# Kernel optimization log

Hardware: AMD Instinct MI355X
Metric: run time of the kernel (lower is better)

## Reference

```python
import jax, jax.numpy as jnp
import numpy as np

N_NODES = 100000
N_EDGES = 1600000
IN_FEATS = 512
HEADS = 8
HID = 8            # out_feats per head of the input layer
N_CLASSES = 40
NEG_SLOPE = 0.2    # DGL GATv2Conv default


def gatv2_layer(h, src, dst, Ws, bs, Wd, bd, attn, n_nodes):
    """One DGL-style GATv2Conv (eval mode: dropouts are identity).
    h: [N, F_in]; Ws/Wd: [F_in, H*D]; attn: [H, D]. Returns [N, H*D]."""
    H, D = attn.shape
    hs = (h @ Ws + bs).reshape(-1, H, D)   # fc_src(h)
    hd = (h @ Wd + bd).reshape(-1, H, D)   # fc_dst(h)
    es = hs[src]                           # [E,H,D] messages (feat_src on edges)
    ed = hd[dst]                           # [E,H,D]
    e = jax.nn.leaky_relu(es + ed, NEG_SLOPE)
    logits = jnp.einsum('ehd,hd->eh', e, attn)          # [E,H]
    # segment softmax over incoming edges of each dst node
    m = jax.ops.segment_max(logits, dst, num_segments=n_nodes)
    m = jnp.where(jnp.isfinite(m), m, 0.0)              # nodes with no in-edges
    p = jnp.exp(logits - m[dst])
    s = jax.ops.segment_sum(p, dst, num_segments=n_nodes)
    alpha = p / (s[dst] + 1e-9)                         # [E,H]
    out = jax.ops.segment_sum(alpha[:, :, None] * es, dst, num_segments=n_nodes)
    return out.reshape(n_nodes, H * D)


def setup_inputs() -> dict:
    key = jax.random.key(0)
    ks = jax.random.split(key, 12)
    x = jax.random.normal(ks[0], (N_NODES, IN_FEATS), dtype=jnp.float32)
    src = jax.random.randint(ks[1], (N_EDGES,), 0, N_NODES, dtype=jnp.int32)
    dst = jax.random.randint(ks[2], (N_EDGES,), 0, N_NODES, dtype=jnp.int32)
    s1 = 1.0 / np.sqrt(IN_FEATS)
    s2 = 1.0 / np.sqrt(HEADS * HID)
    W1s = jax.random.normal(ks[3], (IN_FEATS, HEADS * HID), dtype=jnp.float32) * s1
    W1d = jax.random.normal(ks[4], (IN_FEATS, HEADS * HID), dtype=jnp.float32) * s1
    b1s = jnp.zeros((HEADS * HID,), jnp.float32)
    b1d = jnp.zeros((HEADS * HID,), jnp.float32)
    a1 = jax.random.normal(ks[5], (HEADS, HID), dtype=jnp.float32) * s2
    W2s = jax.random.normal(ks[6], (HEADS * HID, N_CLASSES), dtype=jnp.float32) * s2
    W2d = jax.random.normal(ks[7], (HEADS * HID, N_CLASSES), dtype=jnp.float32) * s2
    b2s = jnp.zeros((N_CLASSES,), jnp.float32)
    b2d = jnp.zeros((N_CLASSES,), jnp.float32)
    a2 = jax.random.normal(ks[8], (1, N_CLASSES), dtype=jnp.float32) * (1.0 / np.sqrt(N_CLASSES))
    return {"x": x, "src": src, "dst": dst,
            "W1s": W1s, "b1s": b1s, "W1d": W1d, "b1d": b1d, "a1": a1,
            "W2s": W2s, "b2s": b2s, "W2d": W2d, "b2d": b2d, "a2": a2}


def reference(x, src, dst, W1s, b1s, W1d, b1d, a1, W2s, b2s, W2d, b2d, a2):
    h = gatv2_layer(x, src, dst, W1s, b1s, W1d, b1d, a1, N_NODES)   # [N, H*HID]
    h = jax.nn.elu(h)
    out = gatv2_layer(h, src, dst, W2s, b2s, W2d, b2d, a2, N_NODES)  # [N, C]
    return out
```

## Files before the change

### kernel.cpp

```cpp
#include <hip/hip_runtime.h>
#include <math.h>

#define N_NODES 100000
#define N_EDGES 1600000
#define F_IN    512
#define HD1     64
#define NHEAD   8
#define NC      40
#define NEG_SLOPE 0.2f

typedef _Float16 h8 __attribute__((ext_vector_type(8)));
typedef _Float16 h4 __attribute__((ext_vector_type(4)));
typedef float f4 __attribute__((ext_vector_type(4)));

__global__ __launch_bounds__(256) void prep_all(
    const float* __restrict__ W1s, const float* __restrict__ W1d,
    _Float16* __restrict__ btgf,
    const float* __restrict__ W2s, const float* __restrict__ W2d,
    _Float16* __restrict__ btg2, int* __restrict__ deg){
  int i = blockIdx.x*256 + threadIdx.x;
  {
    int j = i & 7, lane = (i>>3)&63, t = (i>>9)&7, kstep = i>>12;
    int k = kstep*32 + (lane>>4)*8 + j;
    int n = t*16 + (lane&15);
    float v = (n < 64) ? W1s[k*64 + n] : W1d[k*64 + (n-64)];
    btgf[i] = (_Float16)v;
  }
  if(i < 80*64){
    int n = i >> 6, k = i & 63;
    float v = (n < 40) ? W2s[k*40 + n] : W2d[k*40 + (n-40)];
    btg2[i] = (_Float16)v;
  }
  for(int k=i; k<N_NODES; k+=65536) deg[k] = 0;
}

__global__ __launch_bounds__(256) void hist_dst(const int* __restrict__ dst,
                                                int* __restrict__ deg){
  int xcd = blockIdx.x & 7;
  int lo = xcd*12500, hi = lo + 12500;
  int e0 = (blockIdx.x >> 3)*1024 + threadIdx.x*4;
  if(e0 + 3 < N_EDGES){
    int4 d4 = *(const int4*)&dst[e0];
    if(d4.x >= lo && d4.x < hi) atomicAdd(&deg[d4.x], 1);
    if(d4.y >= lo && d4.y < hi) atomicAdd(&deg[d4.y], 1);
    if(d4.z >= lo && d4.z < hi) atomicAdd(&deg[d4.z], 1);
    if(d4.w >= lo && d4.w < hi) atomicAdd(&deg[d4.w], 1);
  } else {
    for(int j=0;j<4;j++){
      int e = e0 + j;
      if(e < N_EDGES){
        int d = dst[e];
        if(d >= lo && d < hi) atomicAdd(&deg[d], 1);
      }
    }
  }
}

__global__ __launch_bounds__(256) void scan1(const int* __restrict__ deg,
                                             int* __restrict__ row,
                                             int* __restrict__ bsum){
  __shared__ int sm[256];
  int t = threadIdx.x;
  int base = blockIdx.x*1024 + t*4;
  int v0 = base+0<N_NODES ? deg[base+0] : 0;
  int v1 = base+1<N_NODES ? deg[base+1] : 0;
  int v2 = base+2<N_NODES ? deg[base+2] : 0;
  int v3 = base+3<N_NODES ? deg[base+3] : 0;
  int tsum = v0+v1+v2+v3;
  sm[t] = tsum; __syncthreads();
  for(int off=1; off<256; off<<=1){
    int x = (t>=off) ? sm[t-off] : 0;
    __syncthreads();
    sm[t] += x;
    __syncthreads();
  }
  int excl = sm[t] - tsum;
  if(t==255) bsum[blockIdx.x] = sm[255];
  if(base+0<N_NODES) row[base+0] = excl;
  if(base+1<N_NODES) row[base+1] = excl+v0;
  if(base+2<N_NODES) row[base+2] = excl+v0+v1;
  if(base+3<N_NODES) row[base+3] = excl+v0+v1+v2;
}

__global__ __launch_bounds__(128) void scan2(int* __restrict__ bsum, int nb){
  __shared__ int sm[128];
  int t = threadIdx.x;
  int v = (t<nb) ? bsum[t] : 0;
  sm[t] = v; __syncthreads();
  for(int off=1; off<128; off<<=1){
    int x = (t>=off) ? sm[t-off] : 0;
    __syncthreads();
    sm[t] += x;
    __syncthreads();
  }
  if(t<nb) bsum[t] = sm[t] - v;
}

__global__ __launch_bounds__(256) void scan3(int* __restrict__ row,
                                             const int* __restrict__ bsum,
                                             int* __restrict__ cur){
  int i = blockIdx.x*256 + threadIdx.x;
  if(i >= N_NODES) return;
  int r = row[i] + bsum[i>>10];
  row[i] = r; cur[i] = r;
}

__global__ __launch_bounds__(256) void scatter_edges(const int* __restrict__ src,
                                                     const int* __restrict__ dst,
                                                     int* __restrict__ cur,
                                                     int* __restrict__ esrc){
  int xcd = blockIdx.x & 7;
  int lo = xcd*12500, hi = lo + 12500;
  int e0 = (blockIdx.x >> 3)*1024 + threadIdx.x*4;
  if(e0 + 3 < N_EDGES){
    int4 d4 = *(const int4*)&dst[e0];
    int4 s4 = *(const int4*)&src[e0];
    if(d4.x >= lo && d4.x < hi){ int p = atomicAdd(&cur[d4.x],1); esrc[p] = s4.x; }
    if(d4.y >= lo && d4.y < hi){ int p = atomicAdd(&cur[d4.y],1); esrc[p] = s4.y; }
    if(d4.z >= lo && d4.z < hi){ int p = atomicAdd(&cur[d4.z],1); esrc[p] = s4.z; }
    if(d4.w >= lo && d4.w < hi){ int p = atomicAdd(&cur[d4.w],1); esrc[p] = s4.w; }
  } else {
    for(int j=0;j<4;j++){
      int e = e0 + j;
      if(e < N_EDGES){
        int d = dst[e];
        if(d >= lo && d < hi){ int p = atomicAdd(&cur[d],1); esrc[p] = src[e]; }
      }
    }
  }
}

__global__ __launch_bounds__(256,4) void gemm1_mfma(
    const float* __restrict__ x, const _Float16* __restrict__ btgf,
    const float* __restrict__ bs, const float* __restrict__ bd,
    _Float16* __restrict__ hs, _Float16* __restrict__ hd){
  __shared__ _Float16 at[2][64*136];
  int tid = threadIdx.x;
  int lane = tid & 63, w = tid >> 6;
  int l15 = lane & 15, quad = lane >> 4;
  int row0 = blockIdx.x * 64;

  f4 acc[4][2];
  #pragma unroll
  for(int rt=0;rt<4;rt++){ acc[rt][0] = (f4){0.f,0.f,0.f,0.f}; acc[rt][1] = (f4){0.f,0.f,0.f,0.f}; }

  int sr[8], sc4[8];
  #pragma unroll
  for(int j=0;j<8;j++){
    int s = tid + j*256;
    int r = s >> 5, c4 = s & 31;
    int gr = row0 + r; if(gr >= N_NODES) gr = N_NODES-1;
    sr[j] = gr; sc4[j] = c4;
  }

  float4 pf[8];
  #pragma unroll
  for(int j=0;j<8;j++)
    pf[j] = *(const float4*)&x[sr[j]*F_IN + sc4[j]*4];

  for(int kc=0; kc<4; kc++){
    int buf = kc & 1;
    #pragma unroll
    for(int j=0;j<8;j++){
      int s = tid + j*256;
      int r = s >> 5, c4 = s & 31;
      h4 hv;
      hv[0]=(_Float16)pf[j].x; hv[1]=(_Float16)pf[j].y;
      hv[2]=(_Float16)pf[j].z; hv[3]=(_Float16)pf[j].w;
      *(h4*)&at[buf][r*136 + c4*4] = hv;
    }
    if(kc < 3){
      #pragma unroll
      for(int j=0;j<8;j++)
        pf[j] = *(const float4*)&x[sr[j]*F_IN + (kc+1)*128 + sc4[j]*4];
    }
    __syncthreads();
    #pragma unroll
    for(int ks=0;ks<4;ks++){
      int fbase = (((kc*4+ks)*8) + 2*w)*512 + lane*8;
      h8 b0 = *(const h8*)&btgf[fbase];
      h8 b1 = *(const h8*)&btgf[fbase + 512];
      #pragma unroll
      for(int rt=0;rt<4;rt++){
        h8 af = *(const h8*)&at[buf][(rt*16+l15)*136 + ks*32 + quad*8];
        acc[rt][0] = __builtin_amdgcn_mfma_f32_16x16x32_f16(af, b0, acc[rt][0], 0,0,0);
        acc[rt][1] = __builtin_amdgcn_mfma_f32_16x16x32_f16(af, b1, acc[rt][1], 0,0,0);
      }
    }
  }
  #pragma unroll
  for(int tt=0;tt<2;tt++){
    int colg = (2*w+tt)*16 + l15;
    float bv; _Float16* op; int c;
    if(colg < 64){ bv = bs[colg]; op = hs; c = colg; }
    else         { bv = bd[colg-64]; op = hd; c = colg-64; }
    #pragma unroll
    for(int rt=0;rt<4;rt++){
      #pragma unroll
      for(int reg=0;reg<4;reg++){
        int rr = row0 + rt*16 + quad*4 + reg;
        if(rr < N_NODES) op[rr*HD1 + c] = (_Float16)(acc[rt][tt][reg] + bv);
      }
    }
  }
}

__global__ __launch_bounds__(256) void gemm2_mfma(
    const _Float16* __restrict__ h1h, const _Float16* __restrict__ btg,
    const float* __restrict__ bs, const float* __restrict__ bd,
    _Float16* __restrict__ hs2, _Float16* __restrict__ hd2){
  int tid = threadIdx.x;
  int lane = tid & 63, w = tid >> 6;
  int l15 = lane & 15, quad = lane >> 4;
  int rbase = blockIdx.x*192 + w*48;
  h8 bf[2][5];
  #pragma unroll
  for(int ks=0;ks<2;ks++)
    #pragma unroll
    for(int t=0;t<5;t++)
      bf[ks][t] = *(const h8*)&btg[(t*16 + l15)*64 + ks*32 + quad*8];
  f4 acc[3][5];
  #pragma unroll
  for(int mt=0;mt<3;mt++)
    #pragma unroll
    for(int t=0;t<5;t++) acc[mt][t] = (f4){0.f,0.f,0.f,0.f};
  #pragma unroll
  for(int mt=0;mt<3;mt++){
    int r = rbase + mt*16 + l15;
    if(r >= N_NODES) r = N_NODES-1;
    const _Float16* ap = h1h + r*HD1 + quad*8;
    #pragma unroll
    for(int ks=0;ks<2;ks++){
      h8 af = *(const h8*)(ap + ks*32);
      #pragma unroll
      for(int t=0;t<5;t++)
        acc[mt][t] = __builtin_amdgcn_mfma_f32_16x16x32_f16(af, bf[ks][t], acc[mt][t], 0,0,0);
    }
  }
  #pragma unroll
  for(int t=0;t<5;t++){
    int colg = t*16 + l15;
    float bv; _Float16* op; int c;
    if(colg < 40){ bv = bs[colg]; op = hs2; c = colg; }
    else         { bv = bd[colg-40]; op = hd2; c = colg-40; }
    #pragma unroll
    for(int mt=0;mt<3;mt++)
      #pragma unroll
      for(int reg=0;reg<4;reg++){
        int rr = rbase + mt*16 + quad*4 + reg;
        if(rr < N_NODES) op[rr*NC + c] = (_Float16)(acc[mt][t][reg] + bv);
      }
  }
}

__global__ __launch_bounds__(256) void node_attn1(
    const _Float16* __restrict__ hs, const _Float16* __restrict__ hd,
    const int* __restrict__ row, const int* __restrict__ deg,
    const int* __restrict__ esrc, const float* __restrict__ attn,
    _Float16* __restrict__ out){
  int node = blockIdx.x*4 + (threadIdx.x>>6);
  int lane = threadIdx.x & 63;
  if(node >= N_NODES) return;
  int h  = lane & 7;
  int es = lane >> 3;
  h8 hdh = *(const h8*)&hd[node*HD1 + h*8];
  float4 a0 = *(const float4*)&attn[h*8];
  float4 a1 = *(const float4*)&attn[h*8+4];
  float hdv[8], av[8];
  hdv[0]=(float)hdh[0]; hdv[1]=(float)hdh[1]; hdv[2]=(float)hdh[2]; hdv[3]=(float)hdh[3];
  hdv[4]=(float)hdh[4]; hdv[5]=(float)hdh[5]; hdv[6]=(float)hdh[6]; hdv[7]=(float)hdh[7];
  av[0]=a0.x; av[1]=a0.y; av[2]=a0.z; av[3]=a0.w;
  av[4]=a1.x; av[5]=a1.y; av[6]=a1.z; av[7]=a1.w;
  int st = row[node], dg = deg[node];
  float m = -1e30f, sum = 0.f;
  float acc[8] = {0.f,0.f,0.f,0.f,0.f,0.f,0.f,0.f};
  for(int sb = 0; sb < dg; sb += 64){
    int nblk = dg - sb; if(nblk > 64) nblk = 64;
    int li = st + sb + lane;
    int last = st + dg - 1;
    if(li > last) li = last;
    int sv = esrc[li];
    int iters = (nblk + 7) >> 3;
    int s0 = __shfl(sv, es);
    h8 hsh = *(const h8*)&hs[s0*HD1 + h*8];
    for(int i=0;i<iters;i++){
      h8 ch = hsh;
      bool val = (i*8 + es) < nblk;
      if(i+1 < iters){
        int sn = __shfl(sv, (i+1)*8 + es);
        hsh = *(const h8*)&hs[sn*HD1 + h*8];
      }
      float hsv[8]; float t = 0.f;
      #pragma unroll
      for(int j=0;j<8;j++){
        hsv[j] = (float)ch[j];
        float v = hsv[j] + hdv[j];
        v = fmaxf(v, NEG_SLOPE*v);
        t = fmaf(v, av[j], t);
      }
      if(!val) t = -1e30f;
      float mn = fmaxf(m, t);
      float eo = __expf(m - mn);
      float p  = __expf(t - mn);
      sum = sum*eo + p;
      #pragma unroll
      for(int j=0;j<8;j++) acc[j] = fmaf(p, hsv[j], acc[j]*eo);
      m = mn;
    }
  }
  float mg = m;
  mg = fmaxf(mg, __shfl_xor(mg,8));
  mg = fmaxf(mg, __shfl_xor(mg,16));
  mg = fmaxf(mg, __shfl_xor(mg,32));
  float sc = __expf(m - mg);
  sum *= sc;
  sum += __shfl_xor(sum,8); sum += __shfl_xor(sum,16); sum += __shfl_xor(sum,32);
  #pragma unroll
  for(int j=0;j<8;j++){
    acc[j] *= sc;
    acc[j] += __shfl_xor(acc[j],8);
    acc[j] += __shfl_xor(acc[j],16);
    acc[j] += __shfl_xor(acc[j],32);
  }
  if(es == 0){
    float inv = 1.f / (sum + 1e-9f);
    h8 o;
    #pragma unroll
    for(int j=0;j<8;j++){
      float r = acc[j] * inv;
      r = r>0.f ? r : expm1f(r);
      o[j] = (_Float16)r;
    }
    *(h8*)&out[node*HD1 + h*8] = o;
  }
}

__global__ __launch_bounds__(256) void node_attn2(
    const _Float16* __restrict__ hs, const _Float16* __restrict__ hd,
    const int* __restrict__ row, const int* __restrict__ deg,
    const int* __restrict__ esrc, const float* __restrict__ attn,
    float* __restrict__ out){
  int node = blockIdx.x*4 + (threadIdx.x>>6);
  int lane = threadIdx.x & 63;
  if(node >= N_NODES) return;
  int f  = lane & 7;
  int es = lane >> 3;
  bool fact = (f < 5);
  float hdv[8], av[8];
  if(fact){
    h8 hdh = *(const h8*)&hd[node*NC + f*8];
    float4 a0 = *(const float4*)&attn[f*8];
    float4 a1 = *(const float4*)&attn[f*8+4];
    hdv[0]=(float)hdh[0]; hdv[1]=(float)hdh[1]; hdv[2]=(float)hdh[2]; hdv[3]=(float)hdh[3];
    hdv[4]=(float)hdh[4]; hdv[5]=(float)hdh[5]; hdv[6]=(float)hdh[6]; hdv[7]=(float)hdh[7];
    av[0]=a0.x; av[1]=a0.y; av[2]=a0.z; av[3]=a0.w;
    av[4]=a1.x; av[5]=a1.y; av[6]=a1.z; av[7]=a1.w;
  } else {
    #pragma unroll
    for(int j=0;j<8;j++){ hdv[j]=0.f; av[j]=0.f; }
  }
  int st = row[node], dg = deg[node];
  float m = -1e30f, sum = 0.f;
  float acc[8] = {0.f,0.f,0.f,0.f,0.f,0.f,0.f,0.f};
  for(int sb = 0; sb < dg; sb += 64){
    int nblk = dg - sb; if(nblk > 64) nblk = 64;
    int li = st + sb + lane;
    int last = st + dg - 1;
    if(li > last) li = last;
    int sv = esrc[li];
    int iters = (nblk + 7) >> 3;
    int s0 = __shfl(sv, es);
    h8 hsh;
    if(fact) hsh = *(const h8*)&hs[s0*NC + f*8];
    for(int i=0;i<iters;i++){
      h8 ch = hsh;
      bool val = (i*8 + es) < nblk;
      int sn = 0;
      if(i+1 < iters) sn = __shfl(sv, (i+1)*8 + es);
      if(i+1 < iters && fact) hsh = *(const h8*)&hs[sn*NC + f*8];
      float hsv[8]; float t = 0.f;
      if(fact){
        #pragma unroll
        for(int j=0;j<8;j++){
          hsv[j] = (float)ch[j];
          float v = hsv[j] + hdv[j];
          v = fmaxf(v, NEG_SLOPE*v);
          t = fmaf(v, av[j], t);
        }
      } else {
        #pragma unroll
        for(int j=0;j<8;j++) hsv[j] = 0.f;
      }
      t += __shfl_xor(t,1); t += __shfl_xor(t,2); t += __shfl_xor(t,4);
      if(!val) t = -1e30f;
      float mn = fmaxf(m, t);
      float eo = __expf(m - mn);
      float p  = __expf(t - mn);
      sum = sum*eo + p;
      #pragma unroll
      for(int j=0;j<8;j++) acc[j] = fmaf(p, hsv[j], acc[j]*eo);
      m = mn;
    }
  }
  float mg = m;
  mg = fmaxf(mg, __shfl_xor(mg,8));
  mg = fmaxf(mg, __shfl_xor(mg,16));
  mg = fmaxf(mg, __shfl_xor(mg,32));
  float sc = __expf(m - mg);
  sum *= sc;
  sum += __shfl_xor(sum,8); sum += __shfl_xor(sum,16); sum += __shfl_xor(sum,32);
  #pragma unroll
  for(int j=0;j<8;j++){
    acc[j] *= sc;
    acc[j] += __shfl_xor(acc[j],8);
    acc[j] += __shfl_xor(acc[j],16);
    acc[j] += __shfl_xor(acc[j],32);
  }
  if(es == 0 && fact){
    float inv = 1.f / (sum + 1e-9f);
    f4 o0, o1;
    o0[0]=acc[0]*inv; o0[1]=acc[1]*inv; o0[2]=acc[2]*inv; o0[3]=acc[3]*inv;
    o1[0]=acc[4]*inv; o1[1]=acc[5]*inv; o1[2]=acc[6]*inv; o1[3]=acc[7]*inv;
    *(f4*)&out[node*NC + f*8]     = o0;
    *(f4*)&out[node*NC + f*8 + 4] = o1;
  }
}

extern "C" void kernel_launch(void* const* d_in, const int* in_sizes, int n_in,
                              void* d_out, int out_size, void* d_ws, size_t ws_size,
                              hipStream_t stream) {
  const float* x   = (const float*)d_in[0];
  const int*   src = (const int*)  d_in[1];
  const int*   dst = (const int*)  d_in[2];
  const float* W1s = (const float*)d_in[3];
  const float* b1s = (const float*)d_in[4];
  const float* W1d = (const float*)d_in[5];
  const float* b1d = (const float*)d_in[6];
  const float* a1  = (const float*)d_in[7];
  const float* W2s = (const float*)d_in[8];
  const float* b2s = (const float*)d_in[9];
  const float* W2d = (const float*)d_in[10];
  const float* b2d = (const float*)d_in[11];
  const float* a2  = (const float*)d_in[12];
  float* out = (float*)d_out;

  float* ws = (float*)d_ws;
  _Float16* hs1h = (_Float16*)ws;
  _Float16* hd1h = (_Float16*)(ws + 3200000);
  _Float16* h1h  = (_Float16*)(ws + 6400000);
  _Float16* hs2h = (_Float16*)(ws + 9600000);
  _Float16* hd2h = (_Float16*)(ws + 11600000);
  _Float16* btg1 = (_Float16*)(ws + 13600000);
  _Float16* btg2 = (_Float16*)(ws + 13632768);
  int*   deg  = (int*)(ws + 13635328);
  int*   row  = deg  + 100000;
  int*   cur  = row  + 100000;
  int*   bsum = cur  + 100000;
  int*   esrc = bsum + 128;

  dim3 b256(256);
  const int NB = (N_NODES+255)/256;
  const int SB = (N_NODES+1023)/1024;
  const int G1 = (N_NODES+63)/64;
  const int G2 = (N_NODES+191)/192;
  const int XB = ((N_EDGES+1023)/1024)*8;

  prep_all<<<256, b256, 0, stream>>>(W1s, W1d, btg1, W2s, W2d, btg2, deg);

  hist_dst<<<XB, b256, 0, stream>>>(dst, deg);
  scan1<<<SB, b256, 0, stream>>>(deg, row, bsum);
  scan2<<<1, dim3(128), 0, stream>>>(bsum, SB);
  scan3<<<NB, b256, 0, stream>>>(row, bsum, cur);
  scatter_edges<<<XB, b256, 0, stream>>>(src, dst, cur, esrc);

  gemm1_mfma<<<G1, b256, 0, stream>>>(x, btg1, b1s, b1d, hs1h, hd1h);
  node_attn1<<<(N_NODES+3)/4, b256, 0, stream>>>(hs1h, hd1h, row, deg, esrc, a1, h1h);

  gemm2_mfma<<<G2, b256, 0, stream>>>(h1h, btg2, b2s, b2d, hs2h, hd2h);
  node_attn2<<<(N_NODES+3)/4, b256, 0, stream>>>(hs2h, hd2h, row, deg, esrc, a2, out);
}
```

Baseline: 605.4 us.

## Fuse dst histogram into gemm1 launch and merge scan2 into scan3

Interleaves the degree-histogram blocks with the first-layer GEMM blocks in a single launch (one GEMM block per nine) so the atomic histogram overlaps the compute-bound GEMM. Also folds the single-block bsum scan into the final scan kernel, with each block rescanning the 98 block sums itself, removing a launch. The fused kernel carries the GEMM's LDS and register footprint for the histogram blocks, which may reduce their occupancy.

New measurement: 546.9 us. 9.7% less time.

```diff
diff --git a/kernel.cpp b/kernel.cpp
--- a/kernel.cpp
+++ b/kernel.cpp
@@ -34,23 +34,101 @@
   for(int k=i; k<N_NODES; k+=65536) deg[k] = 0;
 }
 
-__global__ __launch_bounds__(256) void hist_dst(const int* __restrict__ dst,
-                                                int* __restrict__ deg){
-  int xcd = blockIdx.x & 7;
-  int lo = xcd*12500, hi = lo + 12500;
-  int e0 = (blockIdx.x >> 3)*1024 + threadIdx.x*4;
-  if(e0 + 3 < N_EDGES){
-    int4 d4 = *(const int4*)&dst[e0];
-    if(d4.x >= lo && d4.x < hi) atomicAdd(&deg[d4.x], 1);
-    if(d4.y >= lo && d4.y < hi) atomicAdd(&deg[d4.y], 1);
-    if(d4.z >= lo && d4.z < hi) atomicAdd(&deg[d4.z], 1);
-    if(d4.w >= lo && d4.w < hi) atomicAdd(&deg[d4.w], 1);
-  } else {
-    for(int j=0;j<4;j++){
-      int e = e0 + j;
-      if(e < N_EDGES){
-        int d = dst[e];
-        if(d >= lo && d < hi) atomicAdd(&deg[d], 1);
+__global__ __launch_bounds__(256,4) void gemm1_hist(
+    const float* __restrict__ x, const _Float16* __restrict__ btgf,
+    const float* __restrict__ bs, const float* __restrict__ bd,
+    _Float16* __restrict__ hs, _Float16* __restrict__ hd,
+    const int* __restrict__ dst, int* __restrict__ deg){
+  __shared__ _Float16 at[2][64*136];
+  int gid = blockIdx.x;
+  int gdiv = gid/9;
+  if(gid - gdiv*9 != 0){
+    int hb = gid - gdiv - 1;
+    int xcd = hb & 7;
+    int lo = xcd*12500, hi = lo + 12500;
+    int e0 = (hb >> 3)*1024 + threadIdx.x*4;
+    if(e0 + 3 < N_EDGES){
+      int4 d4 = *(const int4*)&dst[e0];
+      if(d4.x >= lo && d4.x < hi) atomicAdd(&deg[d4.x], 1);
+      if(d4.y >= lo && d4.y < hi) atomicAdd(&deg[d4.y], 1);
+      if(d4.z >= lo && d4.z < hi) atomicAdd(&deg[d4.z], 1);
+      if(d4.w >= lo && d4.w < hi) atomicAdd(&deg[d4.w], 1);
+    } else {
+      for(int j=0;j<4;j++){
+        int e = e0 + j;
+        if(e < N_EDGES){
+          int d = dst[e];
+          if(d >= lo && d < hi) atomicAdd(&deg[d], 1);
+        }
+      }
+    }
+    return;
+  }
+  int tid = threadIdx.x;
+  int lane = tid & 63, w = tid >> 6;
+  int l15 = lane & 15, quad = lane >> 4;
+  int row0 = gdiv * 64;
+
+  f4 acc[4][2];
+  #pragma unroll
+  for(int rt=0;rt<4;rt++){ acc[rt][0] = (f4){0.f,0.f,0.f,0.f}; acc[rt][1] = (f4){0.f,0.f,0.f,0.f}; }
+
+  int sr[8], sc4[8];
+  #pragma unroll
+  for(int j=0;j<8;j++){
+    int s = tid + j*256;
+    int r = s >> 5, c4 = s & 31;
+    int gr = row0 + r; if(gr >= N_NODES) gr = N_NODES-1;
+    sr[j] = gr; sc4[j] = c4;
+  }
+
+  float4 pf[8];
+  #pragma unroll
+  for(int j=0;j<8;j++)
+    pf[j] = *(const float4*)&x[sr[j]*F_IN + sc4[j]*4];
+
+  for(int kc=0; kc<4; kc++){
+    int buf = kc & 1;
+    #pragma unroll
+    for(int j=0;j<8;j++){
+      int s = tid + j*256;
+      int r = s >> 5, c4 = s & 31;
+      h4 hv;
+      hv[0]=(_Float16)pf[j].x; hv[1]=(_Float16)pf[j].y;
+      hv[2]=(_Float16)pf[j].z; hv[3]=(_Float16)pf[j].w;
+      *(h4*)&at[buf][r*136 + c4*4] = hv;
+    }
+    if(kc < 3){
+      #pragma unroll
+      for(int j=0;j<8;j++)
+        pf[j] = *(const float4*)&x[sr[j]*F_IN + (kc+1)*128 + sc4[j]*4];
+    }
+    __syncthreads();
+    #pragma unroll
+    for(int ks=0;ks<4;ks++){
+      int fbase = (((kc*4+ks)*8) + 2*w)*512 + lane*8;
+      h8 b0 = *(const h8*)&btgf[fbase];
+      h8 b1 = *(const h8*)&btgf[fbase + 512];
+      #pragma unroll
+      for(int rt=0;rt<4;rt++){
+        h8 af = *(const h8*)&at[buf][(rt*16+l15)*136 + ks*32 + quad*8];
+        acc[rt][0] = __builtin_amdgcn_mfma_f32_16x16x32_f16(af, b0, acc[rt][0], 0,0,0);
+        acc[rt][1] = __builtin_amdgcn_mfma_f32_16x16x32_f16(af, b1, acc[rt][1], 0,0,0);
+      }
+    }
+  }
+  #pragma unroll
+  for(int tt=0;tt<2;tt++){
+    int colg = (2*w+tt)*16 + l15;
+    float bv; _Float16* op; int c;
+    if(colg < 64){ bv = bs[colg]; op = hs; c = colg; }
+    else         { bv = bd[colg-64]; op = hd; c = colg-64; }
+    #pragma unroll
+    for(int rt=0;rt<4;rt++){
+      #pragma unroll
+      for(int reg=0;reg<4;reg++){
+        int rr = row0 + rt*16 + quad*4 + reg;
+        if(rr < N_NODES) op[rr*HD1 + c] = (_Float16)(acc[rt][tt][reg] + bv);
       }
     }
   }
@@ -82,27 +160,33 @@
   if(base+3<N_NODES) row[base+3] = excl+v0+v1+v2;
 }
 
-__global__ __launch_bounds__(128) void scan2(int* __restrict__ bsum, int nb){
+#define SB_N 98
+__global__ __launch_bounds__(256) void scan23(int* __restrict__ row,
+                                              const int* __restrict__ bsum,
+                                              int* __restrict__ cur){
   __shared__ int sm[128];
+  __shared__ int sme[128];
   int t = threadIdx.x;
-  int v = (t<nb) ? bsum[t] : 0;
-  sm[t] = v; __syncthreads();
+  int v = 0;
+  if(t < 128){
+    v = (t < SB_N) ? bsum[t] : 0;
+    sm[t] = v;
+  }
+  __syncthreads();
   for(int off=1; off<128; off<<=1){
-    int x = (t>=off) ? sm[t-off] : 0;
+    int x = 0;
+    if(t < 128 && t >= off) x = sm[t-off];
     __syncthreads();
-    sm[t] += x;
+    if(t < 128) sm[t] += x;
     __syncthreads();
   }
-  if(t<nb) bsum[t] = sm[t] - v;
-}
-
-__global__ __launch_bounds__(256) void scan3(int* __restrict__ row,
-                                             const int* __restrict__ bsum,
-                                             int* __restrict__ cur){
-  int i = blockIdx.x*256 + threadIdx.x;
-  if(i >= N_NODES) return;
-  int r = row[i] + bsum[i>>10];
-  row[i] = r; cur[i] = r;
+  if(t < 128) sme[t] = sm[t] - v;
+  __syncthreads();
+  int i = blockIdx.x*256 + t;
+  if(i < N_NODES){
+    int r = row[i] + sme[i>>10];
+    row[i] = r; cur[i] = r;
+  }
 }
 
 __global__ __launch_bounds__(256) void scatter_edges(const int* __restrict__ src,
@@ -125,81 +209,6 @@
       if(e < N_EDGES){
         int d = dst[e];
         if(d >= lo && d < hi){ int p = atomicAdd(&cur[d],1); esrc[p] = src[e]; }
-      }
-    }
-  }
-}
-
-__global__ __launch_bounds__(256,4) void gemm1_mfma(
-    const float* __restrict__ x, const _Float16* __restrict__ btgf,
-    const float* __restrict__ bs, const float* __restrict__ bd,
-    _Float16* __restrict__ hs, _Float16* __restrict__ hd){
-  __shared__ _Float16 at[2][64*136];
-  int tid = threadIdx.x;
-  int lane = tid & 63, w = tid >> 6;
-  int l15 = lane & 15, quad = lane >> 4;
-  int row0 = blockIdx.x * 64;
-
-  f4 acc[4][2];
-  #pragma unroll
-  for(int rt=0;rt<4;rt++){ acc[rt][0] = (f4){0.f,0.f,0.f,0.f}; acc[rt][1] = (f4){0.f,0.f,0.f,0.f}; }
-
-  int sr[8], sc4[8];
-  #pragma unroll
-  for(int j=0;j<8;j++){
-    int s = tid + j*256;
-    int r = s >> 5, c4 = s & 31;
-    int gr = row0 + r; if(gr >= N_NODES) gr = N_NODES-1;
-    sr[j] = gr; sc4[j] = c4;
-  }
-
-  float4 pf[8];
-  #pragma unroll
-  for(int j=0;j<8;j++)
-    pf[j] = *(const float4*)&x[sr[j]*F_IN + sc4[j]*4];
-
-  for(int kc=0; kc<4; kc++){
-    int buf = kc & 1;
-    #pragma unroll
-    for(int j=0;j<8;j++){
-      int s = tid + j*256;
-      int r = s >> 5, c4 = s & 31;
-      h4 hv;
-      hv[0]=(_Float16)pf[j].x; hv[1]=(_Float16)pf[j].y;
-      hv[2]=(_Float16)pf[j].z; hv[3]=(_Float16)pf[j].w;
-      *(h4*)&at[buf][r*136 + c4*4] = hv;
-    }
-    if(kc < 3){
-      #pragma unroll
-      for(int j=0;j<8;j++)
-        pf[j] = *(const float4*)&x[sr[j]*F_IN + (kc+1)*128 + sc4[j]*4];
-    }
-    __syncthreads();
-    #pragma unroll
-    for(int ks=0;ks<4;ks++){
-      int fbase = (((kc*4+ks)*8) + 2*w)*512 + lane*8;
-      h8 b0 = *(const h8*)&btgf[fbase];
-      h8 b1 = *(const h8*)&btgf[fbase + 512];
-      #pragma unroll
-      for(int rt=0;rt<4;rt++){
-        h8 af = *(const h8*)&at[buf][(rt*16+l15)*136 + ks*32 + quad*8];
-        acc[rt][0] = __builtin_amdgcn_mfma_f32_16x16x32_f16(af, b0, acc[rt][0], 0,0,0);
-        acc[rt][1] = __builtin_amdgcn_mfma_f32_16x16x32_f16(af, b1, acc[rt][1], 0,0,0);
-      }
-    }
-  }
-  #pragma unroll
-  for(int tt=0;tt<2;tt++){
-    int colg = (2*w+tt)*16 + l15;
-    float bv; _Float16* op; int c;
-    if(colg < 64){ bv = bs[colg]; op = hs; c = colg; }
-    else         { bv = bd[colg-64]; op = hd; c = colg-64; }
-    #pragma unroll
-    for(int rt=0;rt<4;rt++){
-      #pragma unroll
-      for(int reg=0;reg<4;reg++){
-        int rr = row0 + rt*16 + quad*4 + reg;
-        if(rr < N_NODES) op[rr*HD1 + c] = (_Float16)(acc[rt][tt][reg] + bv);
       }
     }
   }
@@ -464,16 +473,16 @@
   const int G1 = (N_NODES+63)/64;
   const int G2 = (N_NODES+191)/192;
   const int XB = ((N_EDGES+1023)/1024)*8;
+  const int GH = G1 + XB;
 
   prep_all<<<256, b256, 0, stream>>>(W1s, W1d, btg1, W2s, W2d, btg2, deg);
 
-  hist_dst<<<XB, b256, 0, stream>>>(dst, deg);
+  gemm1_hist<<<GH, b256, 0, stream>>>(x, btg1, b1s, b1d, hs1h, hd1h, dst, deg);
+
   scan1<<<SB, b256, 0, stream>>>(deg, row, bsum);
-  scan2<<<1, dim3(128), 0, stream>>>(bsum, SB);
-  scan3<<<NB, b256, 0, stream>>>(row, bsum, cur);
+  scan23<<<NB, b256, 0, stream>>>(row, bsum, cur);
   scatter_edges<<<XB, b256, 0, stream>>>(src, dst, cur, esrc);
 
-  gemm1_mfma<<<G1, b256, 0, stream>>>(x, btg1, b1s, b1d, hs1h, hd1h);
   node_attn1<<<(N_NODES+3)/4, b256, 0, stream>>>(hs1h, hd1h, row, deg, esrc, a1, h1h);
 
   gemm2_mfma<<<G2, b256, 0, stream>>>(h1h, btg2, b2s, b2d, hs2h, hd2h);
```
